# Performance work log

Hardware: AMD Instinct MI355X
Metric: run time of the kernel (lower is better)

Reference implementation:

```python
import jax, jax.numpy as jnp
import numpy as np

EPS = 1e-5
NUM_GROUPS = 32
NUM_HEADS = 4


def setup_inputs() -> dict:
    key = jax.random.key(0)
    ks = jax.random.split(key, 7)
    b, c, h, w = 4, 256, 64, 64
    x = jax.random.normal(ks[0], (b, c, h, w), dtype=jnp.float32)
    gn_w = jax.random.normal(ks[1], (c,), dtype=jnp.float32) * 0.02 + 1.0
    gn_b = jax.random.normal(ks[2], (c,), dtype=jnp.float32) * 0.02
    qkv_w = jax.random.normal(ks[3], (3 * c, c), dtype=jnp.float32) * (1.0 / np.sqrt(c))
    qkv_b = jax.random.normal(ks[4], (3 * c,), dtype=jnp.float32) * 0.02
    proj_w = jax.random.normal(ks[5], (c, c), dtype=jnp.float32) * (1.0 / np.sqrt(c))
    proj_b = jax.random.normal(ks[6], (c,), dtype=jnp.float32) * 0.02
    return {"x": x, "gn_w": gn_w, "gn_b": gn_b, "qkv_w": qkv_w,
            "qkv_b": qkv_b, "proj_w": proj_w, "proj_b": proj_b}


def _group_norm(x, w, b):
    # GroupNorm32: compute in float32, cast back to input dtype
    bsz, c, h, ww = x.shape
    xf = x.astype(jnp.float32).reshape(bsz, NUM_GROUPS, c // NUM_GROUPS, h, ww)
    mean = xf.mean(axis=(2, 3, 4), keepdims=True)
    var = xf.var(axis=(2, 3, 4), keepdims=True)
    xn = (xf - mean) * jax.lax.rsqrt(var + EPS)
    xn = xn.reshape(bsz, c, h, ww)
    xn = xn * w[None, :, None, None] + b[None, :, None, None]
    return xn.astype(x.dtype)


def reference(x, gn_w, gn_b, qkv_w, qkv_b, proj_w, proj_b):
    b, c, h, w = x.shape
    hd = c // NUM_HEADS
    n = h * w
    xn = _group_norm(x, gn_w, gn_b)
    # 1x1 conv == per-pixel linear: [b, 3c, h, w]
    qkv = jnp.einsum('oc,bchw->bohw', qkv_w, xn) + qkv_b[None, :, None, None]
    qkv = qkv.reshape(b, 3, NUM_HEADS, hd, n)
    q, k, v = qkv[:, 0], qkv[:, 1], qkv[:, 2]  # [b, H, hd, n]
    scale = hd ** -0.5
    # scores [b, H, n, n]
    attn = jnp.einsum('bhdq,bhdk->bhqk', q, k) * scale
    attn = jax.nn.softmax(attn, axis=-1)
    out = jnp.einsum('bhqk,bhdk->bhdq', attn, v)  # [b, H, hd, n]
    out = out.reshape(b, c, h, w)
    out = jnp.einsum('oc,bchw->bohw', proj_w, out) + proj_b[None, :, None, None]
    return x + out
```

## Files before the change

### kernel.cpp

```cpp
#include <hip/hip_runtime.h>

typedef __attribute__((ext_vector_type(8))) short bfrag;
typedef __attribute__((ext_vector_type(4))) float ffrag;
typedef __attribute__((ext_vector_type(8))) unsigned short us8;
typedef __attribute__((ext_vector_type(4))) unsigned short us4;
typedef __attribute__((ext_vector_type(2))) unsigned short us2;

#define DEVI static __device__ __forceinline__

DEVI unsigned short f2bf(float f){
  unsigned int u = __float_as_uint(f);
  u += 0x7fffu + ((u >> 16) & 1u);
  return (unsigned short)(u >> 16);
}
DEVI float fexp2(float x){ float r; asm("v_exp_f32 %0, %1" : "=v"(r) : "v"(x)); return r; }
DEVI unsigned int cvt_pk_bf16(float lo, float hi){
  unsigned int r;
  asm("v_cvt_pk_bf16_f32 %0, %1, %2" : "=v"(r) : "v"(lo), "v"(hi));
  return r;
}
DEVI int swz64(int r, int c){ return ((r << 6) + c) ^ ((r & 7) << 3); }
DEVI int swz256(int r, int c){ return ((r << 8) + c) ^ ((r & 7) << 3); }

DEVI void gload16(const unsigned short* g, unsigned short* l){
  __builtin_amdgcn_global_load_lds(
      (const __attribute__((address_space(1))) unsigned int*)g,
      (__attribute__((address_space(3))) unsigned int*)l, 16, 0, 0);
}

__global__ __launch_bounds__(256) void prep_w(
    const float* __restrict__ qkvw, const float* __restrict__ qkvb,
    const float* __restrict__ pw, unsigned short* __restrict__ wq,
    unsigned short* __restrict__ wp, float* __restrict__ bq){
  const int i = blockIdx.x * 256 + threadIdx.x;
  const float qs = 0.125f * 1.44269504f;
  if (i < 49152){
    float4 v = ((const float4*)qkvw)[i];
    float sc = (i < 16384) ? qs : 1.f;
    us4 u; u[0]=f2bf(v.x*sc); u[1]=f2bf(v.y*sc); u[2]=f2bf(v.z*sc); u[3]=f2bf(v.w*sc);
    ((us4*)wq)[i] = u;
  }
  if (i < 16384){
    float4 v = ((const float4*)pw)[i];
    us4 u; u[0]=f2bf(v.x); u[1]=f2bf(v.y); u[2]=f2bf(v.z); u[3]=f2bf(v.w);
    ((us4*)wp)[i] = u;
  }
  if (i < 768) bq[i] = qkvb[i] * (i < 256 ? qs : 1.f);
}

__global__ __launch_bounds__(256) void gn_stats(
    const float* __restrict__ x, const float* __restrict__ gw,
    const float* __restrict__ gb, float* __restrict__ ss){
  const int b = blockIdx.x >> 5, g = blockIdx.x & 31;
  const int t = threadIdx.x;
  const float4* base = (const float4*)(x + (((size_t)b * 256 + g * 8) << 12));
  float s = 0.f, q = 0.f;
  #pragma unroll
  for (int i = 0; i < 32; ++i){
    float4 v = base[i * 256 + t];
    s += v.x + v.y + v.z + v.w;
    q += v.x * v.x + v.y * v.y + v.z * v.z + v.w * v.w;
  }
  #pragma unroll
  for (int m = 32; m; m >>= 1){ s += __shfl_down(s, m); q += __shfl_down(q, m); }
  __shared__ float ps[4], pq[4];
  if ((t & 63) == 0){ ps[t >> 6] = s; pq[t >> 6] = q; }
  __syncthreads();
  if (t < 8){
    float S = ps[0] + ps[1] + ps[2] + ps[3];
    float Q = pq[0] + pq[1] + pq[2] + pq[3];
    float mean = S * (1.f / 32768.f);
    float var  = Q * (1.f / 32768.f) - mean * mean;
    float rstd = rsqrtf(var + 1e-5f);
    int c = g * 8 + t;
    float sc = gw[c] * rstd;
    ss[b * 256 + c] = sc;
    ss[1024 + b * 256 + c] = gb[c] - mean * sc;
  }
}

__global__ __launch_bounds__(256) void normalize_t(
    const float* __restrict__ x, const float* __restrict__ ss,
    unsigned short* __restrict__ xnt){
  const int n0 = blockIdx.x << 6, b = blockIdx.y;
  const int t = threadIdx.x;
  __shared__ unsigned short T[64 * 258];
  const float* xb = x + ((size_t)b << 20);
  const float* sc = ss + b * 256;
  const float* sh = ss + 1024 + b * 256;
  #pragma unroll 4
  for (int e = 0; e < 64; ++e){
    int idx = e * 256 + t;
    int c = idx >> 6, nl = idx & 63;
    float v = xb[((size_t)c << 12) + n0 + nl];
    T[nl * 258 + c] = f2bf(v * sc[c] + sh[c]);
  }
  __syncthreads();
  unsigned short* dst = xnt + ((((size_t)b << 12) + n0) << 8);
  #pragma unroll 4
  for (int e = 0; e < 32; ++e){
    int idx = e * 256 + t;
    int nl = idx >> 7, c2 = (idx & 127) << 1;
    *(us2*)(dst + (nl << 8) + c2) = *(const us2*)&T[nl * 258 + c2];
  }
}

__global__ __launch_bounds__(256) void qkv_gemm(
    const unsigned short* __restrict__ xnt, const unsigned short* __restrict__ W,
    const float* __restrict__ bias, unsigned short* __restrict__ qt,
    unsigned short* __restrict__ kt, unsigned short* __restrict__ vt){
  const int n0 = blockIdx.x << 6, MT = blockIdx.y, b = blockIdx.z;
  const int t = threadIdx.x, l = t & 63, w = t >> 6;
  __shared__ __align__(16) unsigned short Al[64 * 256];
  __shared__ __align__(16) unsigned short Bl[64 * 256];
  const us8* Asrc = (const us8*)(W + (size_t)(MT << 6) * 256);
  #pragma unroll
  for (int e = 0; e < 8; ++e){
    int g = e * 256 + t;
    *(us8*)&Al[swz256(g >> 5, (g & 31) << 3)] = Asrc[g];
  }
  const us8* src = (const us8*)(xnt + ((((size_t)b << 12) + n0) << 8));
  #pragma unroll
  for (int e = 0; e < 8; ++e){
    int g = e * 256 + t;
    *(us8*)&Bl[swz256(g >> 5, (g & 31) << 3)] = src[g];
  }
  __syncthreads();
  ffrag acc[4] = {{0,0,0,0},{0,0,0,0},{0,0,0,0},{0,0,0,0}};
  #pragma unroll
  for (int kc = 0; kc < 8; ++kc){
    bfrag a = *(const bfrag*)&Al[swz256((w << 4) + (l & 15), (kc << 5) + ((l >> 4) << 3))];
    #pragma unroll
    for (int fc = 0; fc < 4; ++fc){
      bfrag bb = *(const bfrag*)&Bl[swz256((fc << 4) + (l & 15), (kc << 5) + ((l >> 4) << 3))];
      acc[fc] = __builtin_amdgcn_mfma_f32_16x16x32_bf16(a, bb, acc[fc], 0, 0, 0);
    }
  }
  const int which = MT >> 2, h = MT & 3;
  const int d0 = (w << 4) + ((l >> 4) << 2);
  float bi[4];
  #pragma unroll
  for (int r = 0; r < 4; ++r) bi[r] = bias[(MT << 6) + d0 + r];
  #pragma unroll
  for (int fc = 0; fc < 4; ++fc){
    int n = n0 + (fc << 4) + (l & 15);
    if (which < 2){
      unsigned short* dst = (which == 0 ? qt : kt) +
          (((size_t)(b * 4 + h)) << 18) + ((size_t)n << 6) + d0;
      us4 u;
      #pragma unroll
      for (int r = 0; r < 4; ++r) u[r] = f2bf(acc[fc][r] + bi[r]);
      *(us4*)dst = u;
    } else {
      const int np = n0 + ((fc & 2) << 4) + (((l >> 2) & 3) << 3)
                        + ((fc & 1) << 2) + (l & 3);
      #pragma unroll
      for (int r = 0; r < 4; ++r)
        vt[((((size_t)(b * 4 + h)) << 6) + d0 + r) * 4096 + np] = f2bf(acc[fc][r] + bi[r]);
    }
  }
}

__global__ __launch_bounds__(512, 4) void attn_kernel(
    const unsigned short* __restrict__ qt, const unsigned short* __restrict__ kt,
    const unsigned short* __restrict__ vt, unsigned short* __restrict__ at){
  const int q0 = blockIdx.x << 7, h = blockIdx.y, b = blockIdx.z;
  const int t = threadIdx.x, l = t & 63, w = t >> 6;
  const int wq = w & 3, kh = w >> 2;
  const size_t bh = (size_t)b * 4 + h;
  __shared__ __align__(16) unsigned short S[16384];
  const unsigned short* kbase = kt + (bh << 18);
  const unsigned short* vbase = vt + (bh << 18);

  const int row = t >> 3;
  const int gx = ((t & 7) ^ (row & 7)) << 3;
  const int koff = (row << 6) + gx;
  unsigned short* ldst = &S[w << 9];
  const unsigned short* qsrc = qt + (bh << 18) + ((size_t)q0 << 6);
  gload16(qsrc + koff, ldst);
  gload16(qsrc + 4096 + koff, ldst + 12288);
  gload16(kbase + koff, ldst + 4096);
  gload16(vbase + (row << 12) + gx, ldst + 8192);
  __syncthreads();
  const int qreg = (wq >> 1) ? 12288 : 0;
  const int qrow = ((wq & 1) << 5) + (l & 15);
  bfrag bq00 = *(const bfrag*)&S[qreg + swz64(qrow,      (l >> 4) << 3)];
  bfrag bq01 = *(const bfrag*)&S[qreg + swz64(qrow, 32 + ((l >> 4) << 3))];
  bfrag bq10 = *(const bfrag*)&S[qreg + swz64(qrow + 16,      (l >> 4) << 3)];
  bfrag bq11 = *(const bfrag*)&S[qreg + swz64(qrow + 16, 32 + ((l >> 4) << 3))];
  __syncthreads();

  ffrag acc[2][4] = {{{0,0,0,0},{0,0,0,0},{0,0,0,0},{0,0,0,0}},
                     {{0,0,0,0},{0,0,0,0},{0,0,0,0},{0,0,0,0}}};
  float m[2] = {-1e30f, -1e30f}, lsum[2] = {0.f, 0.f};

  #pragma unroll 2
  for (int kti = 0; kti < 64; ++kti){
    const int kb = (kti & 1) ? 0 : 4096;
    const int vb = (kti & 1) ? 12288 : 8192;
    if (kti < 63){
      const int kb2 = (kti & 1) ? 4096 : 0;
      const int vb2 = (kti & 1) ? 8192 : 12288;
      gload16(kbase + ((kti + 1) << 12) + koff, ldst + kb2);
      gload16(vbase + (row << 12) + ((kti + 1) << 6) + gx, ldst + vb2);
    }
    ffrag s[2][2];
    __builtin_amdgcn_s_setprio(1);
    #pragma unroll
    for (int j = 0; j < 2; ++j){
      const int fc = (kh << 1) + j;
      bfrag ak0 = *(const bfrag*)&S[kb + swz64((fc << 4) + (l & 15), (l >> 4) << 3)];
      bfrag ak1 = *(const bfrag*)&S[kb + swz64((fc << 4) + (l & 15), 32 + ((l >> 4) << 3))];
      ffrag z0 = {0,0,0,0}, z1 = {0,0,0,0};
      z0 = __builtin_amdgcn_mfma_f32_16x16x32_bf16(ak0, bq00, z0, 0, 0, 0);
      z0 = __builtin_amdgcn_mfma_f32_16x16x32_bf16(ak1, bq01, z0, 0, 0, 0);
      z1 = __builtin_amdgcn_mfma_f32_16x16x32_bf16(ak0, bq10, z1, 0, 0, 0);
      z1 = __builtin_amdgcn_mfma_f32_16x16x32_bf16(ak1, bq11, z1, 0, 0, 0);
      s[0][j] = z0; s[1][j] = z1;
    }
    __builtin_amdgcn_s_setprio(0);
    float p[2][2][4], ps[2];
    #pragma unroll
    for (int g = 0; g < 2; ++g){
      #pragma unroll
      for (int j = 0; j < 2; ++j){
        #pragma unroll
        for (int r = 0; r < 4; ++r) p[g][j][r] = fexp2(s[g][j][r] - m[g]);
      }
      ps[g] = ((p[g][0][0] + p[g][0][1]) + (p[g][0][2] + p[g][0][3])) +
              ((p[g][1][0] + p[g][1][1]) + (p[g][1][2] + p[g][1][3]));
    }
    if (!__all(ps[0] <= 8192.f && ps[1] <= 8192.f)){
      #pragma unroll
      for (int g = 0; g < 2; ++g){
        float lm = fmaxf(fmaxf(s[g][0][0], s[g][0][1]), fmaxf(s[g][0][2], s[g][0][3]));
        lm = fmaxf(lm, fmaxf(fmaxf(s[g][1][0], s[g][1][1]), fmaxf(s[g][1][2], s[g][1][3])));
        float pm = fmaxf(lm, __shfl_xor(lm, 16));
        pm = fmaxf(pm, __shfl_xor(pm, 32));
        float mn = fmaxf(m[g], pm);
        float al = fexp2(m[g] - mn);
        m[g] = mn;
        lsum[g] *= al;
        float alT[4];
        #pragma unroll
        for (int r = 0; r < 4; ++r) alT[r] = __shfl(al, ((l >> 4) << 2) + r);
        #pragma unroll
        for (int fc = 0; fc < 4; ++fc){
          #pragma unroll
          for (int r = 0; r < 4; ++r) acc[g][fc][r] *= alT[r];
        }
        #pragma unroll
        for (int j = 0; j < 2; ++j){
          #pragma unroll
          for (int r = 0; r < 4; ++r) p[g][j][r] = fexp2(s[g][j][r] - m[g]);
        }
        ps[g] = ((p[g][0][0] + p[g][0][1]) + (p[g][0][2] + p[g][0][3])) +
                ((p[g][1][0] + p[g][1][1]) + (p[g][1][2] + p[g][1][3]));
      }
    }
    lsum[0] += ps[0]; lsum[1] += ps[1];
    union { bfrag b; unsigned int u[4]; } A0, A1;
    A0.u[0] = cvt_pk_bf16(p[0][0][0], p[0][0][1]); A0.u[1] = cvt_pk_bf16(p[0][0][2], p[0][0][3]);
    A0.u[2] = cvt_pk_bf16(p[0][1][0], p[0][1][1]); A0.u[3] = cvt_pk_bf16(p[0][1][2], p[0][1][3]);
    A1.u[0] = cvt_pk_bf16(p[1][0][0], p[1][0][1]); A1.u[1] = cvt_pk_bf16(p[1][0][2], p[1][0][3]);
    A1.u[2] = cvt_pk_bf16(p[1][1][0], p[1][1][1]); A1.u[3] = cvt_pk_bf16(p[1][1][2], p[1][1][3]);
    __builtin_amdgcn_s_setprio(1);
    #pragma unroll
    for (int fc = 0; fc < 4; ++fc){
      bfrag vv = *(const bfrag*)&S[vb + swz64((fc << 4) + (l & 15),
                                             (kh << 5) + ((l >> 4) << 3))];
      acc[0][fc] = __builtin_amdgcn_mfma_f32_16x16x32_bf16(A0.b, vv, acc[0][fc], 0, 0, 0);
      acc[1][fc] = __builtin_amdgcn_mfma_f32_16x16x32_bf16(A1.b, vv, acc[1][fc], 0, 0, 0);
    }
    __builtin_amdgcn_s_setprio(0);
    if (kti < 63) __syncthreads();
  }
  __syncthreads();
  #pragma unroll
  for (int g = 0; g < 2; ++g){
    lsum[g] += __shfl_xor(lsum[g], 16);
    lsum[g] += __shfl_xor(lsum[g], 32);
  }
  float* Sf = (float*)S;
  if (kh == 1 && l < 16){
    #pragma unroll
    for (int g = 0; g < 2; ++g){
      Sf[(wq << 5) + (g << 4) + l] = m[g];
      Sf[128 + (wq << 5) + (g << 4) + l] = lsum[g];
    }
  }
  __syncthreads();
  float fat[2], fbt[2];
  if (kh == 0){
    #pragma unroll
    for (int g = 0; g < 2; ++g){
      float mb = Sf[(wq << 5) + (g << 4) + (l & 15)];
      float lb = Sf[128 + (wq << 5) + (g << 4) + (l & 15)];
      float mn = fmaxf(m[g], mb);
      float fa = fexp2(m[g] - mn), fb = fexp2(mb - mn);
      float inv = 1.f / (lsum[g] * fa + lb * fb);
      fat[g] = fa * inv; fbt[g] = fb * inv;
    }
  }
  __syncthreads();
  if (kh == 1){
    #pragma unroll
    for (int g = 0; g < 2; ++g){
      #pragma unroll
      for (int fc = 0; fc < 4; ++fc){
        #pragma unroll
        for (int r = 0; r < 4; ++r)
          Sf[((wq << 5) + (g << 4) + ((l >> 4) << 2) + r) * 64 + (fc << 4) + (l & 15)] =
              acc[g][fc][r];
      }
    }
  }
  __syncthreads();
  if (kh == 0){
    float faT[2][4], fbT[2][4];
    #pragma unroll
    for (int g = 0; g < 2; ++g){
      #pragma unroll
      for (int r = 0; r < 4; ++r){
        faT[g][r] = __shfl(fat[g], ((l >> 4) << 2) + r);
        fbT[g][r] = __shfl(fbt[g], ((l >> 4) << 2) + r);
      }
    }
    #pragma unroll
    for (int g = 0; g < 2; ++g){
      #pragma unroll
      for (int fc = 0; fc < 4; ++fc){
        #pragma unroll
        for (int r = 0; r < 4; ++r){
          const int ql = (wq << 5) + (g << 4) + ((l >> 4) << 2) + r;
          float ob = Sf[ql * 64 + (fc << 4) + (l & 15)];
          float v = acc[g][fc][r] * faT[g][r] + ob * fbT[g][r];
          at[((((size_t)b << 12) + q0 + ql) << 8) + (h << 6) + (fc << 4) + (l & 15)] =
              f2bf(v);
        }
      }
    }
  }
}

__global__ __launch_bounds__(256) void proj_gemm(
    const unsigned short* __restrict__ at, const unsigned short* __restrict__ W,
    const float* __restrict__ bias, const float* __restrict__ x,
    float* __restrict__ out){
  const int n0 = blockIdx.x << 6, MT = blockIdx.y, b = blockIdx.z;
  const int t = threadIdx.x, l = t & 63, w = t >> 6;
  __shared__ __align__(16) unsigned short Al[64 * 256];
  __shared__ __align__(16) unsigned short Bl[64 * 256];
  const us8* Asrc = (const us8*)(W + (size_t)(MT << 6) * 256);
  #pragma unroll
  for (int e = 0; e < 8; ++e){
    int g = e * 256 + t;
    *(us8*)&Al[swz256(g >> 5, (g & 31) << 3)] = Asrc[g];
  }
  const us8* src = (const us8*)(at + ((((size_t)b << 12) + n0) << 8));
  #pragma unroll
  for (int e = 0; e < 8; ++e){
    int g = e * 256 + t;
    *(us8*)&Bl[swz256(g >> 5, (g & 31) << 3)] = src[g];
  }
  __syncthreads();
  ffrag acc[4] = {{0,0,0,0},{0,0,0,0},{0,0,0,0},{0,0,0,0}};
  #pragma unroll
  for (int kc = 0; kc < 8; ++kc){
    bfrag a = *(const bfrag*)&Al[swz256((w << 4) + (l & 15), (kc << 5) + ((l >> 4) << 3))];
    #pragma unroll
    for (int fc = 0; fc < 4; ++fc){
      bfrag bb = *(const bfrag*)&Bl[swz256((fc << 4) + (l & 15), (kc << 5) + ((l >> 4) << 3))];
      acc[fc] = __builtin_amdgcn_mfma_f32_16x16x32_bf16(a, bb, acc[fc], 0, 0, 0);
    }
  }
  const int co = (MT << 6) + (w << 4) + ((l >> 4) << 2);
  #pragma unroll
  for (int fc = 0; fc < 4; ++fc){
    int n = n0 + (fc << 4) + (l & 15);
    #pragma unroll
    for (int r = 0; r < 4; ++r){
      size_t o = (((size_t)b * 256 + co + r) << 12) + n;
      out[o] = acc[fc][r] + bias[co + r] + x[o];
    }
  }
}

extern "C" void kernel_launch(void* const* d_in, const int* in_sizes, int n_in,
                              void* d_out, int out_size, void* d_ws, size_t ws_size,
                              hipStream_t stream){
  const float* x    = (const float*)d_in[0];
  const float* gw   = (const float*)d_in[1];
  const float* gb   = (const float*)d_in[2];
  const float* qkvw = (const float*)d_in[3];
  const float* qkvb = (const float*)d_in[4];
  const float* pw   = (const float*)d_in[5];
  const float* pb   = (const float*)d_in[6];
  float* out = (float*)d_out;

  float* ss = (float*)d_ws;
  unsigned short* xnt = (unsigned short*)((char*)d_ws + 16384);
  unsigned short* qt  = xnt + (size_t)4 * 4096 * 256;
  unsigned short* kt  = qt  + (size_t)16 * 4096 * 64;
  unsigned short* vt  = kt  + (size_t)16 * 4096 * 64;
  unsigned short* at  = vt  + (size_t)16 * 4096 * 64;
  unsigned short* wq  = at  + (size_t)4 * 4096 * 256;
  unsigned short* wp  = wq  + (size_t)768 * 256;
  float*          bq  = (float*)(wp + (size_t)256 * 256);

  prep_w     <<<256, 256, 0, stream>>>(qkvw, qkvb, pw, wq, wp, bq);
  gn_stats   <<<128, 256, 0, stream>>>(x, gw, gb, ss);
  normalize_t<<<dim3(64, 4), 256, 0, stream>>>(x, ss, xnt);
  qkv_gemm   <<<dim3(64, 12, 4), 256, 0, stream>>>(xnt, wq, bq, qt, kt, vt);
  attn_kernel<<<dim3(32, 4, 4), 512, 0, stream>>>(qt, kt, vt, at);
  proj_gemm  <<<dim3(64, 4, 4), 256, 0, stream>>>(at, wp, pb, x, out);
}
```

Baseline: 128.2 us.

## Triple-buffer K/V loads, fold max subtraction into MFMA init, remap blocks for XCDs

Moves the attention kernel's K/V staging from double to triple buffering in LDS, prefetching two tiles ahead. Barriers become explicit s_waitcnt vmcnt plus s_barrier, so a wait only covers the older load. The running max is now folded into the MFMA accumulator's initial value, which removes the per-element subtraction before exp2. The grid is flattened to 1D with an XCD-aware mapping so that each chiplet handles the same batch/head pairs and reuses K/V in its L2. In exchange the kernel uses more LDS per block, which may lower occupancy, and correctness now depends on hand-written wait counts.

Measured after the change: 126.8 us. About the same (-1.0%).

```diff
diff --git a/kernel.cpp b/kernel.cpp
--- a/kernel.cpp
+++ b/kernel.cpp
@@ -164,11 +164,16 @@
 __global__ __launch_bounds__(512, 4) void attn_kernel(
     const unsigned short* __restrict__ qt, const unsigned short* __restrict__ kt,
     const unsigned short* __restrict__ vt, unsigned short* __restrict__ at){
-  const int q0 = blockIdx.x << 7, h = blockIdx.y, b = blockIdx.z;
+  const int id = blockIdx.x;
+  const int xc = id & 7, k2 = id >> 3;
+  const int bhid = (xc << 1) + (k2 >> 5);
+  const int qx = k2 & 31;
+  const int b = bhid >> 2, h = bhid & 3;
+  const int q0 = qx << 7;
   const int t = threadIdx.x, l = t & 63, w = t >> 6;
   const int wq = w & 3, kh = w >> 2;
-  const size_t bh = (size_t)b * 4 + h;
-  __shared__ __align__(16) unsigned short S[16384];
+  const size_t bh = (size_t)bhid;
+  __shared__ __align__(16) unsigned short S[24576];
   const unsigned short* kbase = kt + (bh << 18);
   const unsigned short* vbase = vt + (bh << 18);
 
@@ -177,41 +182,46 @@
   const int koff = (row << 6) + gx;
   unsigned short* ldst = &S[w << 9];
   const unsigned short* qsrc = qt + (bh << 18) + ((size_t)q0 << 6);
-  gload16(qsrc + koff, ldst);
-  gload16(qsrc + 4096 + koff, ldst + 12288);
-  gload16(kbase + koff, ldst + 4096);
-  gload16(vbase + (row << 12) + gx, ldst + 8192);
-  __syncthreads();
-  const int qreg = (wq >> 1) ? 12288 : 0;
+  gload16(qsrc + koff, ldst + 8192);
+  gload16(qsrc + 4096 + koff, ldst + 20480);
+  gload16(kbase + koff, ldst);
+  gload16(vbase + (row << 12) + gx, ldst + 12288);
+  gload16(kbase + 4096 + koff, ldst + 4096);
+  gload16(vbase + (row << 12) + 64 + gx, ldst + 16384);
+  asm volatile("s_waitcnt vmcnt(2)" ::: "memory");
+  __builtin_amdgcn_s_barrier();
+  __builtin_amdgcn_sched_barrier(0);
+  const int qreg = (wq >> 1) ? 20480 : 8192;
   const int qrow = ((wq & 1) << 5) + (l & 15);
   bfrag bq00 = *(const bfrag*)&S[qreg + swz64(qrow,      (l >> 4) << 3)];
   bfrag bq01 = *(const bfrag*)&S[qreg + swz64(qrow, 32 + ((l >> 4) << 3))];
   bfrag bq10 = *(const bfrag*)&S[qreg + swz64(qrow + 16,      (l >> 4) << 3)];
   bfrag bq11 = *(const bfrag*)&S[qreg + swz64(qrow + 16, 32 + ((l >> 4) << 3))];
-  __syncthreads();
+  asm volatile("s_waitcnt lgkmcnt(0)" ::: "memory");
+  __builtin_amdgcn_s_barrier();
+  __builtin_amdgcn_sched_barrier(0);
 
   ffrag acc[2][4] = {{{0,0,0,0},{0,0,0,0},{0,0,0,0},{0,0,0,0}},
                      {{0,0,0,0},{0,0,0,0},{0,0,0,0},{0,0,0,0}}};
-  float m[2] = {-1e30f, -1e30f}, lsum[2] = {0.f, 0.f};
-
-  #pragma unroll 2
+  float m[2] = {0.f, 0.f}, lsum[2] = {0.f, 0.f};
+
+  int rb = 0, wb = 2;
   for (int kti = 0; kti < 64; ++kti){
-    const int kb = (kti & 1) ? 0 : 4096;
-    const int vb = (kti & 1) ? 12288 : 8192;
-    if (kti < 63){
-      const int kb2 = (kti & 1) ? 4096 : 0;
-      const int vb2 = (kti & 1) ? 8192 : 12288;
-      gload16(kbase + ((kti + 1) << 12) + koff, ldst + kb2);
-      gload16(vbase + (row << 12) + ((kti + 1) << 6) + gx, ldst + vb2);
+    const int kbr = rb << 12, vbr = 12288 + (rb << 12);
+    if (kti <= 61){
+      gload16(kbase + ((kti + 2) << 12) + koff, ldst + (wb << 12));
+      gload16(vbase + (row << 12) + ((kti + 2) << 6) + gx,
+              ldst + 12288 + (wb << 12));
     }
     ffrag s[2][2];
     __builtin_amdgcn_s_setprio(1);
     #pragma unroll
     for (int j = 0; j < 2; ++j){
       const int fc = (kh << 1) + j;
-      bfrag ak0 = *(const bfrag*)&S[kb + swz64((fc << 4) + (l & 15), (l >> 4) << 3)];
-      bfrag ak1 = *(const bfrag*)&S[kb + swz64((fc << 4) + (l & 15), 32 + ((l >> 4) << 3))];
-      ffrag z0 = {0,0,0,0}, z1 = {0,0,0,0};
+      bfrag ak0 = *(const bfrag*)&S[kbr + swz64((fc << 4) + (l & 15), (l >> 4) << 3)];
+      bfrag ak1 = *(const bfrag*)&S[kbr + swz64((fc << 4) + (l & 15), 32 + ((l >> 4) << 3))];
+      ffrag z0 = {-m[0], -m[0], -m[0], -m[0]};
+      ffrag z1 = {-m[1], -m[1], -m[1], -m[1]};
       z0 = __builtin_amdgcn_mfma_f32_16x16x32_bf16(ak0, bq00, z0, 0, 0, 0);
       z0 = __builtin_amdgcn_mfma_f32_16x16x32_bf16(ak1, bq01, z0, 0, 0, 0);
       z1 = __builtin_amdgcn_mfma_f32_16x16x32_bf16(ak0, bq10, z1, 0, 0, 0);
@@ -225,7 +235,7 @@
       #pragma unroll
       for (int j = 0; j < 2; ++j){
         #pragma unroll
-        for (int r = 0; r < 4; ++r) p[g][j][r] = fexp2(s[g][j][r] - m[g]);
+        for (int r = 0; r < 4; ++r) p[g][j][r] = fexp2(s[g][j][r]);
       }
       ps[g] = ((p[g][0][0] + p[g][0][1]) + (p[g][0][2] + p[g][0][3])) +
               ((p[g][1][0] + p[g][1][1]) + (p[g][1][2] + p[g][1][3]));
@@ -237,9 +247,9 @@
         lm = fmaxf(lm, fmaxf(fmaxf(s[g][1][0], s[g][1][1]), fmaxf(s[g][1][2], s[g][1][3])));
         float pm = fmaxf(lm, __shfl_xor(lm, 16));
         pm = fmaxf(pm, __shfl_xor(pm, 32));
-        float mn = fmaxf(m[g], pm);
-        float al = fexp2(m[g] - mn);
-        m[g] = mn;
+        float dm = fmaxf(pm, 0.f);
+        float al = fexp2(-dm);
+        m[g] += dm;
         lsum[g] *= al;
         float alT[4];
         #pragma unroll
@@ -252,7 +262,7 @@
         #pragma unroll
         for (int j = 0; j < 2; ++j){
           #pragma unroll
-          for (int r = 0; r < 4; ++r) p[g][j][r] = fexp2(s[g][j][r] - m[g]);
+          for (int r = 0; r < 4; ++r) p[g][j][r] = fexp2(s[g][j][r] - dm);
         }
         ps[g] = ((p[g][0][0] + p[g][0][1]) + (p[g][0][2] + p[g][0][3])) +
                 ((p[g][1][0] + p[g][1][1]) + (p[g][1][2] + p[g][1][3]));
@@ -267,13 +277,20 @@
     __builtin_amdgcn_s_setprio(1);
     #pragma unroll
     for (int fc = 0; fc < 4; ++fc){
-      bfrag vv = *(const bfrag*)&S[vb + swz64((fc << 4) + (l & 15),
-                                             (kh << 5) + ((l >> 4) << 3))];
+      bfrag vv = *(const bfrag*)&S[vbr + swz64((fc << 4) + (l & 15),
+                                              (kh << 5) + ((l >> 4) << 3))];
       acc[0][fc] = __builtin_amdgcn_mfma_f32_16x16x32_bf16(A0.b, vv, acc[0][fc], 0, 0, 0);
       acc[1][fc] = __builtin_amdgcn_mfma_f32_16x16x32_bf16(A1.b, vv, acc[1][fc], 0, 0, 0);
     }
     __builtin_amdgcn_s_setprio(0);
-    if (kti < 63) __syncthreads();
+    if (kti < 63){
+      if (kti <= 61) asm volatile("s_waitcnt vmcnt(2)" ::: "memory");
+      else           asm volatile("s_waitcnt vmcnt(0)" ::: "memory");
+      __builtin_amdgcn_s_barrier();
+      __builtin_amdgcn_sched_barrier(0);
+    }
+    rb = (rb == 2) ? 0 : rb + 1;
+    wb = (wb == 2) ? 0 : wb + 1;
   }
   __syncthreads();
   #pragma unroll
@@ -285,8 +302,8 @@
   if (kh == 1 && l < 16){
     #pragma unroll
     for (int g = 0; g < 2; ++g){
-      Sf[(wq << 5) + (g << 4) + l] = m[g];
-      Sf[128 + (wq << 5) + (g << 4) + l] = lsum[g];
+      Sf[8192 + (wq << 5) + (g << 4) + l] = m[g];
+      Sf[8448 + (wq << 5) + (g << 4) + l] = lsum[g];
     }
   }
   __syncthreads();
@@ -294,8 +311,8 @@
   if (kh == 0){
     #pragma unroll
     for (int g = 0; g < 2; ++g){
-      float mb = Sf[(wq << 5) + (g << 4) + (l & 15)];
-      float lb = Sf[128 + (wq << 5) + (g << 4) + (l & 15)];
+      float mb = Sf[8192 + (wq << 5) + (g << 4) + (l & 15)];
+      float lb = Sf[8448 + (wq << 5) + (g << 4) + (l & 15)];
       float mn = fmaxf(m[g], mb);
       float fa = fexp2(m[g] - mn), fb = fexp2(mb - mn);
       float inv = 1.f / (lsum[g] * fa + lb * fb);
@@ -412,6 +429,6 @@
   gn_stats   <<<128, 256, 0, stream>>>(x, gw, gb, ss);
   normalize_t<<<dim3(64, 4), 256, 0, stream>>>(x, ss, xnt);
   qkv_gemm   <<<dim3(64, 12, 4), 256, 0, stream>>>(xnt, wq, bq, qt, kt, vt);
-  attn_kernel<<<dim3(32, 4, 4), 512, 0, stream>>>(qt, kt, vt, at);
+  attn_kernel<<<dim3(512), 512, 0, stream>>>(qt, kt, vt, at);
   proj_gemm  <<<dim3(64, 4, 4), 256, 0, stream>>>(at, wp, pb, x, out);
 }
```
